# Performance work log

Hardware: AMD Instinct MI355X
Metric: run time of the kernel (lower is better)

The kernel has to match this reference:

```python
import jax, jax.numpy as jnp
import numpy as np

ALPHA_F, GAMMA_F = 0.25, 2.0   # focal loss params
SMOOTH = 1e-6                  # dice smooth
THETA = 5.0                    # boundary weight
W_FOCAL, W_DICE, W_BOUND = 0.3, 0.4, 0.3


def _erode(m):
    # one iteration of scipy binary_erosion, cross (connectivity-1) structure,
    # border_value=0 (outside treated as False)
    p = jnp.pad(m, ((0, 0), (0, 0), (1, 1), (1, 1)), constant_values=False)
    c = p[:, :, 1:-1, 1:-1]
    up = p[:, :, :-2, 1:-1]
    dn = p[:, :, 2:, 1:-1]
    lf = p[:, :, 1:-1, :-2]
    rt = p[:, :, 1:-1, 2:]
    return c & up & dn & lf & rt


def _dilate(m):
    # one iteration of scipy binary_dilation, cross structure, border_value=0
    p = jnp.pad(m, ((0, 0), (0, 0), (1, 1), (1, 1)), constant_values=False)
    c = p[:, :, 1:-1, 1:-1]
    up = p[:, :, :-2, 1:-1]
    dn = p[:, :, 2:, 1:-1]
    lf = p[:, :, 1:-1, :-2]
    rt = p[:, :, 1:-1, 2:]
    return c | up | dn | lf | rt


def setup_inputs() -> dict:
    key = jax.random.key(0)
    k1, k2 = jax.random.split(key)
    B, C, H, W = 64, 1, 512, 512
    inputs = jax.random.normal(k1, (B, C, H, W), dtype=jnp.float32)
    targets = jax.random.randint(k2, (B, C, H, W), 0, 2).astype(jnp.float32)
    return {"inputs": inputs, "targets": targets}


def reference(inputs, targets):
    # numerically stable BCE-with-logits, elementwise
    bce = jnp.maximum(inputs, 0.0) - inputs * targets + jnp.log1p(jnp.exp(-jnp.abs(inputs)))

    # --- focal loss ---
    pt = jnp.exp(-bce)
    focal_loss = jnp.mean(ALPHA_F * (1.0 - pt) ** GAMMA_F * bce)

    # --- dice loss ---
    p = jax.nn.sigmoid(inputs)
    intersection = jnp.sum(p * targets)
    dice = (2.0 * intersection + SMOOTH) / (jnp.sum(p) + jnp.sum(targets) + SMOOTH)
    dice_loss = 1.0 - dice

    # --- boundary-weighted BCE ---
    mask = targets > 0.5
    eroded = _erode(_erode(mask))      # iterations=2
    dilated = _dilate(_dilate(mask))   # iterations=2
    boundary = dilated & (~eroded)
    weights = boundary.astype(jnp.float32) * THETA + 1.0
    boundary_loss = jnp.mean(bce * weights)

    return W_FOCAL * focal_loss + W_DICE * dice_loss + W_BOUND * boundary_loss
```

## Files before the change

kernel.cpp:

```cpp
#include <hip/hip_runtime.h>
#include <math.h>

static constexpr int Hdim = 512;
static constexpr int Wdim = 512;
static constexpr int HW   = Hdim * Wdim;
static constexpr int NIMG = 64;
static constexpr int WPR  = Wdim / 64;
static constexpr int RSTRIP = 32;
static constexpr int SPI  = Hdim / RSTRIP;
static constexpr int NBLK = NIMG * SPI;
static constexpr int MROWS = RSTRIP + 4;
static constexpr int NGRP  = MROWS * (Wdim / 4);
static constexpr int GPT   = NGRP / 256;
static constexpr int NWORDS = MROWS * WPR;
static constexpr int NIT = (RSTRIP * Wdim) / (256 * 4);


__device__ __forceinline__ unsigned long long shl1(unsigned long long c, unsigned long long l) {
    return (c << 1) | (l >> 63);
}
__device__ __forceinline__ unsigned long long shr1(unsigned long long c, unsigned long long r) {
    return (c >> 1) | (r << 63);
}
__device__ __forceinline__ unsigned long long shl2(unsigned long long c, unsigned long long l) {
    return (c << 2) | (l >> 62);
}
__device__ __forceinline__ unsigned long long shr2(unsigned long long c, unsigned long long r) {
    return (c >> 2) | (r << 62);
}

__global__ __launch_bounds__(256) void fused_loss_kernel(
    const float* __restrict__ inp, const float* __restrict__ tgt,
    float* __restrict__ partials)
{
    __shared__ unsigned int nibw[NGRP / 4];
    __shared__ unsigned long long tmask[MROWS][WPR];
    __shared__ unsigned long long bmask[RSTRIP][WPR];
    __shared__ float smem[4][5];

    const int img   = blockIdx.x / SPI;
    const int strip = blockIdx.x % SPI;
    const int r0    = strip * RSTRIP;
    const float* ib = inp + img * HW;
    const float* tb = tgt + img * HW;

    const int wave = threadIdx.x >> 6;
    const int lane = threadIdx.x & 63;

    const float* base = ib + r0 * Wdim + threadIdx.x * 4;
    float4 cur = *(const float4*)(base);

    unsigned char* nib = (unsigned char*)nibw;
    #pragma unroll 6
    for (int i = 0; i < GPT; i++) {
        int g   = threadIdx.x + i * 256;
        int row = g >> 7;
        int c4  = g & 127;
        int gr  = r0 - 2 + row;
        unsigned int n = 0u;
        if ((unsigned)gr < (unsigned)Hdim) {
            float4 v = *(const float4*)(tb + gr * Wdim + c4 * 4);
            n = (unsigned int)(v.x > 0.5f)
              | ((unsigned int)(v.y > 0.5f) << 1)
              | ((unsigned int)(v.z > 0.5f) << 2)
              | ((unsigned int)(v.w > 0.5f) << 3);
        }
        nib[g] = (unsigned char)n;
    }
    __syncthreads();

    for (int w = threadIdx.x; w < NWORDS; w += 256) {
        unsigned long long word = 0ULL;
        #pragma unroll
        for (int k = 0; k < 4; k++) {
            unsigned int v = nibw[w * 4 + k];
            unsigned int y = v | (v >> 4);
            unsigned int z = y & 0x00FF00FFu;
            unsigned int h = (z | (z >> 8)) & 0xFFFFu;
            word |= (unsigned long long)h << (16 * k);
        }
        tmask[w >> 3][w & 7] = word;
    }
    __syncthreads();

    {
        int row  = threadIdx.x >> 3;
        int word = threadIdx.x & 7;
        int mr = row + 2;

        #define CW(r)  tmask[r][word]
        #define LW(r)  (word > 0 ? tmask[r][word - 1] : 0ULL)
        #define RW(r)  (word < WPR - 1 ? tmask[r][word + 1] : 0ULL)
        unsigned long long c0 = CW(mr),   l0 = LW(mr),   rr0 = RW(mr);
        unsigned long long cm = CW(mr-1), lm = LW(mr-1), rm  = RW(mr-1);
        unsigned long long cp = CW(mr+1), lp = LW(mr+1), rp  = RW(mr+1);
        unsigned long long cm2 = CW(mr-2);
        unsigned long long cp2 = CW(mr+2);
        #undef CW
        #undef LW
        #undef RW

        unsigned long long er =
            c0 & shl1(c0,l0) & shr1(c0,rr0) & shl2(c0,l0) & shr2(c0,rr0)
               & cm & shl1(cm,lm) & shr1(cm,rm)
               & cp & shl1(cp,lp) & shr1(cp,rp)
               & cm2 & cp2;
        unsigned long long di =
            c0 | shl1(c0,l0) | shr1(c0,rr0) | shl2(c0,l0) | shr2(c0,rr0)
               | cm | shl1(cm,lm) | shr1(cm,rm)
               | cp | shl1(cp,lp) | shr1(cp,rp)
               | cm2 | cp2;
        bmask[row][word] = di & ~er;
    }
    __syncthreads();

    float s_focal = 0.f, s_inter = 0.f, s_p = 0.f, s_bw = 0.f;
    int s_tc = 0;

    #pragma unroll
    for (int it = 0; it < NIT; it++) {
        float4 nxt;
        if (it + 1 < NIT) nxt = *(const float4*)(base + (it + 1) * 1024);

        int flat = it * 1024 + threadIdx.x * 4;
        int row  = flat >> 9;
        int x    = flat & (Wdim - 1);
        unsigned int tb4 = (unsigned int)((tmask[row + 2][x >> 6] >> (x & 63)) & 0xFULL);
        unsigned int bb4 = (unsigned int)((bmask[row][x >> 6]     >> (x & 63)) & 0xFULL);
        s_tc += __popc(tb4);
        const float xs[4] = {cur.x, cur.y, cur.z, cur.w};
        #pragma unroll
        for (int k = 0; k < 4; k++) {
            float xi = xs[k];
            bool tpos = (tb4 >> k) & 1;
            float e  = __expf(-fabsf(xi));
            float bce = fmaxf(xi, 0.f) - (tpos ? xi : 0.f) + __logf(1.f + e);
            float rden = __builtin_amdgcn_rcpf(1.f + e);
            float p = (xi >= 0.f ? 1.f : e) * rden;
            float pt = tpos ? p : 1.f - p;
            float om = 1.f - pt;
            s_focal += 0.25f * om * om * bce;
            s_p     += p;
            s_inter += tpos ? p : 0.f;
            float wgt = ((bb4 >> k) & 1) ? 6.0f : 1.0f;
            s_bw += bce * wgt;
        }
        cur = nxt;
    }
    float s_t = (float)s_tc;

    #pragma unroll
    for (int off = 32; off > 0; off >>= 1) {
        s_focal += __shfl_down(s_focal, off);
        s_inter += __shfl_down(s_inter, off);
        s_p     += __shfl_down(s_p,     off);
        s_t     += __shfl_down(s_t,     off);
        s_bw    += __shfl_down(s_bw,    off);
    }
    if (lane == 0) {
        smem[wave][0] = s_focal; smem[wave][1] = s_inter; smem[wave][2] = s_p;
        smem[wave][3] = s_t;     smem[wave][4] = s_bw;
    }
    __syncthreads();
    if (threadIdx.x < 5) {
        float a = smem[0][threadIdx.x] + smem[1][threadIdx.x]
                + smem[2][threadIdx.x] + smem[3][threadIdx.x];
        partials[blockIdx.x * 8 + threadIdx.x] = a;
    }
}

__global__ __launch_bounds__(256) void finalize_kernel(
    const float* __restrict__ partials, float* __restrict__ out)
{
    __shared__ float smem[4][5];
    float a0 = 0.f, a1 = 0.f, a2 = 0.f, a3 = 0.f, a4 = 0.f;
    for (int b = threadIdx.x; b < NBLK; b += 256) {
        const float* s = partials + b * 8;
        a0 += s[0]; a1 += s[1]; a2 += s[2]; a3 += s[3]; a4 += s[4];
    }
    #pragma unroll
    for (int off = 32; off > 0; off >>= 1) {
        a0 += __shfl_down(a0, off);
        a1 += __shfl_down(a1, off);
        a2 += __shfl_down(a2, off);
        a3 += __shfl_down(a3, off);
        a4 += __shfl_down(a4, off);
    }
    int wave = threadIdx.x >> 6;
    int lane = threadIdx.x & 63;
    if (lane == 0) {
        smem[wave][0] = a0; smem[wave][1] = a1; smem[wave][2] = a2;
        smem[wave][3] = a3; smem[wave][4] = a4;
    }
    __syncthreads();
    if (threadIdx.x == 0) {
        double b0 = 0, b1 = 0, b2 = 0, b3 = 0, b4 = 0;
        #pragma unroll
        for (int w = 0; w < 4; w++) {
            b0 += smem[w][0]; b1 += smem[w][1]; b2 += smem[w][2];
            b3 += smem[w][3]; b4 += smem[w][4];
        }
        double invN = 1.0 / (double)(NIMG * HW);
        double focal_loss = b0 * invN;
        double dice = (2.0 * b1 + 1e-6) / (b2 + b3 + 1e-6);
        double boundary_loss = b4 * invN;
        out[0] = (float)(0.3 * focal_loss + 0.4 * (1.0 - dice) + 0.3 * boundary_loss);
    }
}

extern "C" void kernel_launch(void* const* d_in, const int* in_sizes, int n_in,
                              void* d_out, int out_size, void* d_ws, size_t ws_size,
                              hipStream_t stream) {
    const float* inp = (const float*)d_in[0];
    const float* tgt = (const float*)d_in[1];
    float* out = (float*)d_out;
    float* partials = (float*)d_ws;

    fused_loss_kernel<<<NBLK, 256, 0, stream>>>(inp, tgt, partials);
    finalize_kernel<<<1, 256, 0, stream>>>(partials, out);
}
```

Before: 150.2 us.

## Halve row strip height, raise occupancy bound, and prefetch all input loads early

Halves the row strip per block from 32 to 16, which doubles the block count. It adds a launch-bounds occupancy hint of 8 blocks per CU. The first four input float4 loads are issued before the target mask is built, and the remaining four are issued ahead of compute, so more memory requests are in flight to hide latency. In exchange, the 2-row halo is a larger share of each smaller strip, so more target data is re-read, and only half the threads do the boundary-mask step.

Result: no change. 152.3 us (+1.4%).

```diff
diff --git a/kernel.cpp b/kernel.cpp
--- a/kernel.cpp
+++ b/kernel.cpp
@@ -6,7 +6,7 @@
 static constexpr int HW   = Hdim * Wdim;
 static constexpr int NIMG = 64;
 static constexpr int WPR  = Wdim / 64;
-static constexpr int RSTRIP = 32;
+static constexpr int RSTRIP = 16;
 static constexpr int SPI  = Hdim / RSTRIP;
 static constexpr int NBLK = NIMG * SPI;
 static constexpr int MROWS = RSTRIP + 4;
@@ -29,7 +29,7 @@
     return (c >> 2) | (r << 62);
 }
 
-__global__ __launch_bounds__(256) void fused_loss_kernel(
+__global__ __launch_bounds__(256, 8) void fused_loss_kernel(
     const float* __restrict__ inp, const float* __restrict__ tgt,
     float* __restrict__ partials)
 {
@@ -48,10 +48,13 @@
     const int lane = threadIdx.x & 63;
 
     const float* base = ib + r0 * Wdim + threadIdx.x * 4;
-    float4 cur = *(const float4*)(base);
+    float4 b0 = *(const float4*)(base + 0 * 1024);
+    float4 b1 = *(const float4*)(base + 1 * 1024);
+    float4 b2 = *(const float4*)(base + 2 * 1024);
+    float4 b3 = *(const float4*)(base + 3 * 1024);
 
     unsigned char* nib = (unsigned char*)nibw;
-    #pragma unroll 6
+    #pragma unroll
     for (int i = 0; i < GPT; i++) {
         int g   = threadIdx.x + i * 256;
         int row = g >> 7;
@@ -83,7 +86,7 @@
     }
     __syncthreads();
 
-    {
+    if (threadIdx.x < RSTRIP * WPR) {
         int row  = threadIdx.x >> 3;
         int word = threadIdx.x & 7;
         int mr = row + 2;
@@ -117,18 +120,14 @@
     float s_focal = 0.f, s_inter = 0.f, s_p = 0.f, s_bw = 0.f;
     int s_tc = 0;
 
-    #pragma unroll
-    for (int it = 0; it < NIT; it++) {
-        float4 nxt;
-        if (it + 1 < NIT) nxt = *(const float4*)(base + (it + 1) * 1024);
-
+    auto px4 = [&](int it, float4 v) {
         int flat = it * 1024 + threadIdx.x * 4;
         int row  = flat >> 9;
         int x    = flat & (Wdim - 1);
         unsigned int tb4 = (unsigned int)((tmask[row + 2][x >> 6] >> (x & 63)) & 0xFULL);
         unsigned int bb4 = (unsigned int)((bmask[row][x >> 6]     >> (x & 63)) & 0xFULL);
         s_tc += __popc(tb4);
-        const float xs[4] = {cur.x, cur.y, cur.z, cur.w};
+        const float xs[4] = {v.x, v.y, v.z, v.w};
         #pragma unroll
         for (int k = 0; k < 4; k++) {
             float xi = xs[k];
@@ -145,8 +144,21 @@
             float wgt = ((bb4 >> k) & 1) ? 6.0f : 1.0f;
             s_bw += bce * wgt;
         }
-        cur = nxt;
-    }
+    };
+
+    float4 n0 = *(const float4*)(base + 4 * 1024);
+    float4 n1 = *(const float4*)(base + 5 * 1024);
+    px4(0, b0);
+    float4 n2 = *(const float4*)(base + 6 * 1024);
+    px4(1, b1);
+    float4 n3 = *(const float4*)(base + 7 * 1024);
+    px4(2, b2);
+    px4(3, b3);
+    px4(4, n0);
+    px4(5, n1);
+    px4(6, n2);
+    px4(7, n3);
+
     float s_t = (float)s_tc;
 
     #pragma unroll
```

## Halve strip height and issue all target and input loads upfront

Applied to the files above, without the earlier changes.

Reduces the row strip per block from 32 to 16 rows, doubling block count. Every target and logit float4 for the strip is loaded into registers before any shared-memory work, replacing the one-ahead prefetch, so many loads are outstanding at once. A launch-bounds occupancy hint is added. In exchange the halo rows re-read grow relative to useful rows, and register pressure rises.

New measurement: 152.0 us. Within noise of the previous version (+1.2%).

```diff
diff --git a/kernel.cpp b/kernel.cpp
--- a/kernel.cpp
+++ b/kernel.cpp
@@ -6,7 +6,7 @@
 static constexpr int HW   = Hdim * Wdim;
 static constexpr int NIMG = 64;
 static constexpr int WPR  = Wdim / 64;
-static constexpr int RSTRIP = 32;
+static constexpr int RSTRIP = 16;
 static constexpr int SPI  = Hdim / RSTRIP;
 static constexpr int NBLK = NIMG * SPI;
 static constexpr int MROWS = RSTRIP + 4;
@@ -29,7 +29,7 @@
     return (c >> 2) | (r << 62);
 }
 
-__global__ __launch_bounds__(256) void fused_loss_kernel(
+__global__ __launch_bounds__(256, 4) void fused_loss_kernel(
     const float* __restrict__ inp, const float* __restrict__ tgt,
     float* __restrict__ partials)
 {
@@ -47,24 +47,30 @@
     const int wave = threadIdx.x >> 6;
     const int lane = threadIdx.x & 63;
 
+    float4 t[GPT];
+    #pragma unroll
+    for (int i = 0; i < GPT; i++) {
+        int g  = threadIdx.x + i * 256;
+        int gr = r0 - 2 + (g >> 7);
+        t[i] = make_float4(0.f, 0.f, 0.f, 0.f);
+        if ((unsigned)gr < (unsigned)Hdim)
+            t[i] = *(const float4*)(tb + gr * Wdim + (g & 127) * 4);
+    }
     const float* base = ib + r0 * Wdim + threadIdx.x * 4;
-    float4 cur = *(const float4*)(base);
+    float4 b[NIT];
+    #pragma unroll
+    for (int it = 0; it < NIT; it++)
+        b[it] = *(const float4*)(base + it * 1024);
+    asm volatile("" ::: "memory");
 
     unsigned char* nib = (unsigned char*)nibw;
-    #pragma unroll 6
+    #pragma unroll
     for (int i = 0; i < GPT; i++) {
-        int g   = threadIdx.x + i * 256;
-        int row = g >> 7;
-        int c4  = g & 127;
-        int gr  = r0 - 2 + row;
-        unsigned int n = 0u;
-        if ((unsigned)gr < (unsigned)Hdim) {
-            float4 v = *(const float4*)(tb + gr * Wdim + c4 * 4);
-            n = (unsigned int)(v.x > 0.5f)
-              | ((unsigned int)(v.y > 0.5f) << 1)
-              | ((unsigned int)(v.z > 0.5f) << 2)
-              | ((unsigned int)(v.w > 0.5f) << 3);
-        }
+        int g = threadIdx.x + i * 256;
+        unsigned int n = (unsigned int)(t[i].x > 0.5f)
+                       | ((unsigned int)(t[i].y > 0.5f) << 1)
+                       | ((unsigned int)(t[i].z > 0.5f) << 2)
+                       | ((unsigned int)(t[i].w > 0.5f) << 3);
         nib[g] = (unsigned char)n;
     }
     __syncthreads();
@@ -83,7 +89,7 @@
     }
     __syncthreads();
 
-    {
+    if (threadIdx.x < RSTRIP * WPR) {
         int row  = threadIdx.x >> 3;
         int word = threadIdx.x & 7;
         int mr = row + 2;
@@ -119,16 +125,14 @@
 
     #pragma unroll
     for (int it = 0; it < NIT; it++) {
-        float4 nxt;
-        if (it + 1 < NIT) nxt = *(const float4*)(base + (it + 1) * 1024);
-
+        float4 v = b[it];
         int flat = it * 1024 + threadIdx.x * 4;
         int row  = flat >> 9;
         int x    = flat & (Wdim - 1);
         unsigned int tb4 = (unsigned int)((tmask[row + 2][x >> 6] >> (x & 63)) & 0xFULL);
         unsigned int bb4 = (unsigned int)((bmask[row][x >> 6]     >> (x & 63)) & 0xFULL);
         s_tc += __popc(tb4);
-        const float xs[4] = {cur.x, cur.y, cur.z, cur.w};
+        const float xs[4] = {v.x, v.y, v.z, v.w};
         #pragma unroll
         for (int k = 0; k < 4; k++) {
             float xi = xs[k];
@@ -145,7 +149,6 @@
             float wgt = ((bb4 >> k) & 1) ? 6.0f : 1.0f;
             s_bw += bce * wgt;
         }
-        cur = nxt;
     }
     float s_t = (float)s_tc;
 
```
